# Kernel tuning notes

Hardware: AMD Instinct MI355X
Metric: run time of the kernel (lower is better)

Reference implementation:

```python
import jax, jax.numpy as jnp
import numpy as np

Q_HEADS, KV_HEADS, HEAD_DIM, WINDOW = 16, 4, 128, 512
HIDDEN = 2048
ROPE_BASE = 10000.0


def _rope_tables(T, head_dim, dtype):
    half = head_dim // 2
    inv_freq = 1.0 / (ROPE_BASE ** (jnp.arange(half, dtype=jnp.float32) / half))
    t = jnp.arange(T, dtype=jnp.float32)
    freqs = jnp.outer(t, inv_freq)  # [T, half]
    return jnp.cos(freqs).astype(dtype), jnp.sin(freqs).astype(dtype)


def _apply_rope(x, cos, sin):
    # x: [B, T, H, D]; cos/sin: [T, D//2] -> broadcast [1, T, 1, D//2]
    c = cos[None, :, None, :]
    s = sin[None, :, None, :]
    x1, x2 = jnp.split(x, 2, axis=-1)
    return jnp.concatenate([x1 * c - x2 * s, x1 * s + x2 * c], axis=-1)


def setup_inputs() -> dict:
    key = jax.random.key(0)
    ks = jax.random.split(key, 5)
    B, T = 1, 4096
    x = jax.random.normal(ks[0], (B, T, HIDDEN), dtype=jnp.float32)
    sc = 0.02
    wq = jax.random.normal(ks[1], (Q_HEADS * HEAD_DIM, HIDDEN), dtype=jnp.float32) * sc
    wk = jax.random.normal(ks[2], (KV_HEADS * HEAD_DIM, HIDDEN), dtype=jnp.float32) * sc
    wv = jax.random.normal(ks[3], (KV_HEADS * HEAD_DIM, HIDDEN), dtype=jnp.float32) * sc
    wo = jax.random.normal(ks[4], (HIDDEN, Q_HEADS * HEAD_DIM), dtype=jnp.float32) * sc
    return {"x": x, "wq": wq, "wk": wk, "wv": wv, "wo": wo}


def reference(x, wq, wk, wv, wo):
    B, T, _ = x.shape
    reps = Q_HEADS // KV_HEADS
    scale = 1.0 / np.sqrt(HEAD_DIM)

    q = jnp.einsum('bth,oh->bto', x, wq).reshape(B, T, Q_HEADS, HEAD_DIM)
    k = jnp.einsum('bth,oh->bto', x, wk).reshape(B, T, KV_HEADS, HEAD_DIM)
    v = jnp.einsum('bth,oh->bto', x, wv).reshape(B, T, KV_HEADS, HEAD_DIM)

    cos, sin = _rope_tables(T, HEAD_DIM, x.dtype)
    q = _apply_rope(q, cos, sin)
    k = _apply_rope(k, cos, sin)

    # GQA without materializing repeated K/V: group q as [B,T,KVH,reps,D]
    qg = q.reshape(B, T, KV_HEADS, reps, HEAD_DIM)
    scores = jnp.einsum('btgrd,bsgd->bgrts', qg, k) * scale  # [B,KVH,reps,T,T]

    idx = jnp.arange(T)
    # allowed: causal (s <= t) AND within window (t - s <= WINDOW)
    allowed = (idx[None, :] <= idx[:, None]) & (idx[:, None] - idx[None, :] <= WINDOW)
    scores = jnp.where(allowed[None, None, None], scores, jnp.finfo(scores.dtype).min)
    probs = jax.nn.softmax(scores, axis=-1)

    out = jnp.einsum('bgrts,bsgd->btgrd', probs, v)  # [B,T,KVH,reps,D]
    out = out.reshape(B, T, Q_HEADS * HEAD_DIM)
    return jnp.einsum('bto,ho->bth', out, wo)
```

## Files before the change

### kernel.cpp

```cpp
#include <hip/hip_runtime.h>

typedef __attribute__((ext_vector_type(8))) short short8;
typedef __attribute__((ext_vector_type(4))) short short4_t;
typedef __attribute__((ext_vector_type(4))) float f32x4;
typedef __attribute__((ext_vector_type(4))) unsigned short u16x4;

__device__ __forceinline__ unsigned short f2b(float f) {
  unsigned int u = __float_as_uint(f);
  u += 0x7fffu + ((u >> 16) & 1u);
  return (unsigned short)(u >> 16);
}
__device__ __forceinline__ float b2f(unsigned short s) {
  return __uint_as_float(((unsigned int)s) << 16);
}
__device__ __forceinline__ void glds16(const void* g, void* l) {
  __builtin_amdgcn_global_load_lds(
      (const __attribute__((address_space(1))) unsigned int*)g,
      (__attribute__((address_space(3))) unsigned int*)l, 16, 0, 0);
}

__global__ __launch_bounds__(256) void cast_all(const float* __restrict__ x,
                                                const float* __restrict__ wq,
                                                const float* __restrict__ wk,
                                                const float* __restrict__ wv,
                                                const float* __restrict__ wo,
                                                unsigned short* __restrict__ dst) {
  const int i = blockIdx.x * 256 + threadIdx.x;
  const float* s;
  int off;
  if (i < 2097152)      { s = x;  off = i; }
  else if (i < 3145728) { s = wq; off = i - 2097152; }
  else if (i < 3407872) { s = wk; off = i - 3145728; }
  else if (i < 3670016) { s = wv; off = i - 3407872; }
  else                  { s = wo; off = i - 3670016; }
  f32x4 v = ((const f32x4*)s)[off];
  u16x4 o;
  o[0] = f2b(v[0]); o[1] = f2b(v[1]); o[2] = f2b(v[2]); o[3] = f2b(v[3]);
  ((u16x4*)dst)[i] = o;
}

__global__ __launch_bounds__(256) void gemm_qkv(const unsigned short* __restrict__ A,
                                                const unsigned short* __restrict__ B,
                                                unsigned short* __restrict__ qb,
                                                unsigned short* __restrict__ kb,
                                                unsigned short* __restrict__ vtg) {
  const int K = 2048;
  __shared__ unsigned short As[128 * 32];
  __shared__ unsigned short Bs[128 * 32];
  const int tid = threadIdx.x;
  const int w = tid >> 6, lane = tid & 63;
  const int quad = lane >> 4, l15 = lane & 15;
  const int m0 = blockIdx.x * 128;
  const int nt = blockIdx.y;
  const int n0 = nt * 128;
  const int mbase = (w >> 1) * 64;
  const f32x4 fzero = {0.f, 0.f, 0.f, 0.f};

  f32x4 acc[4][4];
#pragma unroll
  for (int i = 0; i < 4; i++)
#pragma unroll
    for (int j = 0; j < 4; j++) acc[i][j] = fzero;

  const int srow = w * 16 + (lane >> 2);
  const int scol = (lane & 3) * 8;
  const unsigned short* Ag0 = A + (size_t)(m0 + srow) * K + scol;
  const unsigned short* Ag1 = Ag0 + (size_t)64 * K;
  const unsigned short* Bg0 = B + (size_t)(n0 + srow) * K + scol;
  const unsigned short* Bg1 = Bg0 + (size_t)64 * K;

  for (int k0 = 0; k0 < K; k0 += 32) {
    __syncthreads();
    glds16(Ag0 + k0, &As[w * 512]);
    glds16(Ag1 + k0, &As[2048 + w * 512]);
    glds16(Bg0 + k0, &Bs[w * 512]);
    glds16(Bg1 + k0, &Bs[2048 + w * 512]);
    __syncthreads();
    short8 af[4], bf[4];
#pragma unroll
    for (int mi = 0; mi < 4; mi++)
      af[mi] = *(const short8*)&As[(mbase + mi * 16 + l15) * 32 + quad * 8];
#pragma unroll
    for (int ni = 0; ni < 4; ni++) {
      const int ngrp = (w & 1) * 2 + (ni & 1) + (ni >> 1) * 4;
      bf[ni] = *(const short8*)&Bs[(ngrp * 16 + l15) * 32 + quad * 8];
    }
#pragma unroll
    for (int mi = 0; mi < 4; mi++)
#pragma unroll
      for (int ni = 0; ni < 4; ni++)
        acc[mi][ni] = __builtin_amdgcn_mfma_f32_16x16x32_bf16(af[mi], bf[ni], acc[mi][ni], 0, 0, 0);
  }

  if (nt >= 20) {
    const int g = nt - 20;
#pragma unroll
    for (int mi = 0; mi < 4; mi++) {
      const int tb = m0 + mbase + mi * 16 + quad * 4;
#pragma unroll
      for (int ni = 0; ni < 4; ni++) {
        const int d = ((w & 1) * 2 + (ni & 1) + (ni >> 1) * 4) * 16 + l15;
        u16x4 o;
#pragma unroll
        for (int r = 0; r < 4; r++) o[r] = f2b(acc[mi][ni][r]);
        *(u16x4*)(vtg + (size_t)(g * 128 + d) * 4096 + tb) = o;
      }
    }
  } else {
    unsigned short* dst;
    int stride, hoff;
    if (nt < 16) { dst = qb; stride = 2048; hoff = nt * 128; }
    else         { dst = kb; stride = 512;  hoff = (nt - 16) * 128; }
    const float c2 = 0.20762050593045889f;
    const float inv2pi = 0.15915494309189535f;
#pragma unroll
    for (int ni = 0; ni < 2; ni++) {
      const int i = (w & 1) * 32 + ni * 16 + l15;
      const float inv_rev = exp2f(-(float)i * c2) * inv2pi;
#pragma unroll
      for (int mi = 0; mi < 4; mi++) {
#pragma unroll
        for (int r = 0; r < 4; r++) {
          const int t = m0 + mbase + mi * 16 + quad * 4 + r;
          float rev = (float)t * inv_rev;
          rev = rev - floorf(rev);
          const float sn = __builtin_amdgcn_sinf(rev);
          const float cs = __builtin_amdgcn_cosf(rev);
          const float x1 = acc[mi][ni][r], x2 = acc[mi][ni + 2][r];
          unsigned short* p = dst + (size_t)t * stride + hoff + i;
          p[0]  = f2b(x1 * cs - x2 * sn);
          p[64] = f2b(x1 * sn + x2 * cs);
        }
      }
    }
  }
}

__global__ __launch_bounds__(256) void gemm_bt(const unsigned short* __restrict__ A,
                                               const unsigned short* __restrict__ B,
                                               float* __restrict__ Cout,
                                               int M, int N, int K) {
  __shared__ unsigned short As[128 * 32];
  __shared__ unsigned short Bs[128 * 32];
  const int tid = threadIdx.x;
  const int w = tid >> 6, lane = tid & 63;
  const int quad = lane >> 4, l15 = lane & 15;
  const int m0 = blockIdx.x * 128, n0 = blockIdx.y * 128;
  const int mbase = (w >> 1) * 64, nbase = (w & 1) * 64;
  const f32x4 fzero = {0.f, 0.f, 0.f, 0.f};

  f32x4 acc[4][4];
#pragma unroll
  for (int i = 0; i < 4; i++)
#pragma unroll
    for (int j = 0; j < 4; j++) acc[i][j] = fzero;

  const int srow = w * 16 + (lane >> 2);
  const int scol = (lane & 3) * 8;
  const unsigned short* Ag0 = A + (size_t)(m0 + srow) * K + scol;
  const unsigned short* Ag1 = Ag0 + (size_t)64 * K;
  const unsigned short* Bg0 = B + (size_t)(n0 + srow) * K + scol;
  const unsigned short* Bg1 = Bg0 + (size_t)64 * K;

  for (int k0 = 0; k0 < K; k0 += 32) {
    __syncthreads();
    glds16(Ag0 + k0, &As[w * 512]);
    glds16(Ag1 + k0, &As[2048 + w * 512]);
    glds16(Bg0 + k0, &Bs[w * 512]);
    glds16(Bg1 + k0, &Bs[2048 + w * 512]);
    __syncthreads();
    short8 af[4], bf[4];
#pragma unroll
    for (int mi = 0; mi < 4; mi++)
      af[mi] = *(const short8*)&As[(mbase + mi * 16 + l15) * 32 + quad * 8];
#pragma unroll
    for (int ni = 0; ni < 4; ni++)
      bf[ni] = *(const short8*)&Bs[(nbase + ni * 16 + l15) * 32 + quad * 8];
#pragma unroll
    for (int mi = 0; mi < 4; mi++)
#pragma unroll
      for (int ni = 0; ni < 4; ni++)
        acc[mi][ni] = __builtin_amdgcn_mfma_f32_16x16x32_bf16(af[mi], bf[ni], acc[mi][ni], 0, 0, 0);
  }

#pragma unroll
  for (int mi = 0; mi < 4; mi++)
#pragma unroll
    for (int ni = 0; ni < 4; ni++) {
      const int row = m0 + mbase + mi * 16 + quad * 4;
      const int col = n0 + nbase + ni * 16 + l15;
#pragma unroll
      for (int r = 0; r < 4; r++)
        Cout[(size_t)(row + r) * N + col] = acc[mi][ni][r];
    }
}

__global__ __launch_bounds__(512) void attn_fwd(const unsigned short* __restrict__ qp,
                                                const unsigned short* __restrict__ kp,
                                                const unsigned short* __restrict__ vtg,
                                                unsigned short* __restrict__ op) {
  __shared__ unsigned short Ks[2][4][1024];
  __shared__ unsigned short Vt[2][4096];
  const int tid = threadIdx.x;
  const int w = tid >> 6, lane = tid & 63;
  const int quad = lane >> 4, l15 = lane & 15;
  const int t0 = blockIdx.x * 64;
  const int g = blockIdx.y;
  const int h = g * 4 + (w & 3);
  const int t0w = t0 + (w >> 2) * 32;
  const f32x4 fzero = {0.f, 0.f, 0.f, 0.f};
  const float scale = 0.088388347648318447f;
  const float NEG_INF = -__builtin_inff();

  short8 qf[4][2];
#pragma unroll
  for (int qt = 0; qt < 2; qt++) {
    const unsigned short* qrow = qp + (size_t)(t0w + qt * 16 + l15) * 2048 + h * 128 + quad * 8;
#pragma unroll
    for (int kb = 0; kb < 4; kb++) qf[kb][qt] = *(const short8*)(qrow + kb * 32);
  }

  f32x4 oacc[8][2];
#pragma unroll
  for (int db = 0; db < 8; db++) { oacc[db][0] = fzero; oacc[db][1] = fzero; }
  float Mrow[2] = {-1.0e30f, -1.0e30f}, Lrow[2] = {0.f, 0.f};

  const int s_begin = (t0 >= 512) ? (t0 - 512) : 0;
  const int nch = ((t0 + 63 - s_begin) >> 5) + 1;

  const int r4 = lane >> 2, c4 = lane & 3;
#define ATTN_STAGE(s0_, b_)                                                              \
  {                                                                                      \
    const int s0v = (s0_);                                                               \
    if (w < 4) {                                                                         \
      _Pragma("unroll")                                                                  \
      for (int p = 0; p < 2; p++)                                                        \
        glds16(kp + (size_t)(s0v + p * 16 + r4) * 512 + g * 128 + w * 32 + c4 * 8,       \
               &Ks[b_][w][p * 512]);                                                     \
    } else {                                                                             \
      const int wv = w - 4;                                                              \
      _Pragma("unroll")                                                                  \
      for (int p = 0; p < 2; p++)                                                        \
        glds16(vtg + (size_t)(g * 128 + wv * 32 + p * 16 + r4) * 4096 + s0v + c4 * 8,    \
               &Vt[b_][wv * 1024 + p * 512]);                                            \
    }                                                                                    \
  }

  ATTN_STAGE(s_begin, 0);

  for (int c = 0; c < nch; ++c) {
    const int s0 = s_begin + c * 32;
    const int b = c & 1;
    __syncthreads();
    if (c + 1 < nch) ATTN_STAGE(s_begin + (c + 1) * 32, (c + 1) & 1);

    if (s0 + 31 >= t0w - 512 && s0 <= t0w + 31) {
      f32x4 sacc[2][2];
      sacc[0][0] = fzero; sacc[0][1] = fzero; sacc[1][0] = fzero; sacc[1][1] = fzero;
      const int permBase = ((l15 >> 2) << 3) + (l15 & 3);
#pragma unroll
      for (int kb = 0; kb < 4; kb++) {
        short8 af0 = *(const short8*)&Ks[b][kb][(permBase + 0) * 32 + quad * 8];
        short8 af1 = *(const short8*)&Ks[b][kb][(permBase + 4) * 32 + quad * 8];
        sacc[0][0] = __builtin_amdgcn_mfma_f32_16x16x32_bf16(af0, qf[kb][0], sacc[0][0], 0, 0, 0);
        sacc[0][1] = __builtin_amdgcn_mfma_f32_16x16x32_bf16(af0, qf[kb][1], sacc[0][1], 0, 0, 0);
        sacc[1][0] = __builtin_amdgcn_mfma_f32_16x16x32_bf16(af1, qf[kb][0], sacc[1][0], 0, 0, 0);
        sacc[1][1] = __builtin_amdgcn_mfma_f32_16x16x32_bf16(af1, qf[kb][1], sacc[1][1], 0, 0, 0);
      }

      short8 pb[2];
      float alpha[2];
#pragma unroll
      for (int qt = 0; qt < 2; qt++) {
        const int tq = t0w + qt * 16 + l15;
        float vals[8];
        float cmax = NEG_INF;
#pragma unroll
        for (int kt = 0; kt < 2; kt++)
#pragma unroll
          for (int r = 0; r < 4; r++) {
            const int s = s0 + quad * 8 + kt * 4 + r;
            const bool ok = (unsigned)(tq - s) <= 512u;
            const float v = ok ? sacc[kt][qt][r] * scale : NEG_INF;
            vals[kt * 4 + r] = v;
            cmax = fmaxf(cmax, v);
          }
        cmax = fmaxf(cmax, __shfl_xor(cmax, 16));
        cmax = fmaxf(cmax, __shfl_xor(cmax, 32));
        const float Mnew = fmaxf(Mrow[qt], cmax);
        alpha[qt] = __expf(Mrow[qt] - Mnew);
        Mrow[qt] = Mnew;
        float csum = 0.f;
#pragma unroll
        for (int j = 0; j < 8; j++) {
          const float p = __expf(vals[j] - Mnew);
          csum += p;
          pb[qt][j] = (short)f2b(p);
        }
        csum += __shfl_xor(csum, 16);
        csum += __shfl_xor(csum, 32);
        Lrow[qt] = Lrow[qt] * alpha[qt] + csum;
      }

#pragma unroll
      for (int db = 0; db < 8; db++) {
        short8 vf = *(const short8*)&Vt[b][(db * 16 + l15) * 32 + quad * 8];
#pragma unroll
        for (int qt = 0; qt < 2; qt++) {
          oacc[db][qt][0] *= alpha[qt]; oacc[db][qt][1] *= alpha[qt];
          oacc[db][qt][2] *= alpha[qt]; oacc[db][qt][3] *= alpha[qt];
          oacc[db][qt] = __builtin_amdgcn_mfma_f32_16x16x32_bf16(vf, pb[qt], oacc[db][qt], 0, 0, 0);
        }
      }
    }
  }
#undef ATTN_STAGE

#pragma unroll
  for (int qt = 0; qt < 2; qt++) {
    const float invL = 1.f / Lrow[qt];
    unsigned short* orow = op + (size_t)(t0w + qt * 16 + l15) * 2048 + h * 128;
#pragma unroll
    for (int db = 0; db < 8; db++) {
      u16x4 o;
#pragma unroll
      for (int r = 0; r < 4; r++) o[r] = f2b(oacc[db][qt][r] * invL);
      *(u16x4*)(orow + db * 16 + quad * 4) = o;
    }
  }
}

extern "C" void kernel_launch(void* const* d_in, const int* in_sizes, int n_in,
                              void* d_out, int out_size, void* d_ws, size_t ws_size,
                              hipStream_t stream) {
  const float* x  = (const float*)d_in[0];
  const float* wq = (const float*)d_in[1];
  const float* wk = (const float*)d_in[2];
  const float* wv = (const float*)d_in[3];
  const float* wo = (const float*)d_in[4];
  float* out = (float*)d_out;
  char* ws = (char*)d_ws;

  unsigned short* xb    = (unsigned short*)(ws + 0);
  unsigned short* wqkv  = (unsigned short*)(ws + 16777216);
  unsigned short* wob   = (unsigned short*)(ws + 29360128);
  unsigned short* qb    = (unsigned short*)(ws + 37748736);
  unsigned short* kbuf  = (unsigned short*)(ws + 54525952);
  unsigned short* vtg   = (unsigned short*)(ws + 58720256);
  unsigned short* attnb = xb;

  cast_all<<<18432, 256, 0, stream>>>(x, wq, wk, wv, wo, (unsigned short*)ws);

  gemm_qkv<<<dim3(32, 24), 256, 0, stream>>>(xb, wqkv, qb, kbuf, vtg);

  attn_fwd<<<dim3(64, 4), 512, 0, stream>>>(qb, kbuf, vtg, attnb);

  gemm_bt<<<dim3(32, 16), 256, 0, stream>>>(attnb, wob, out, 4096, 2048, 2048);
}
```

Baseline: 284.6 us.

## Replace both GEMMs with a 256x256 double-buffered, swizzled, prioritized MFMA kernel

The separate 128x128 QKV and output-projection GEMMs are replaced by one 256x256-tile, 512-thread kernel. It double-buffers 64-wide K slices in 128KB of dynamic LDS, XOR-swizzles the LDS layout to avoid bank conflicts, and interleaves global-to-LDS staging with MFMA quadrants using s_setprio and split barriers. The goal is to hide memory latency and raise data reuse per block. In exchange the grids shrink to 192 and 128 blocks, which may underfill the GPU's compute units, and register pressure rises with 32 accumulators per lane.

```diff
diff --git a/kernel.cpp b/kernel.cpp
--- a/kernel.cpp
+++ b/kernel.cpp
@@ -1,7 +1,6 @@
 #include <hip/hip_runtime.h>
 
 typedef __attribute__((ext_vector_type(8))) short short8;
-typedef __attribute__((ext_vector_type(4))) short short4_t;
 typedef __attribute__((ext_vector_type(4))) float f32x4;
 typedef __attribute__((ext_vector_type(4))) unsigned short u16x4;
 
@@ -9,9 +8,6 @@
   unsigned int u = __float_as_uint(f);
   u += 0x7fffu + ((u >> 16) & 1u);
   return (unsigned short)(u >> 16);
-}
-__device__ __forceinline__ float b2f(unsigned short s) {
-  return __uint_as_float(((unsigned int)s) << 16);
 }
 __device__ __forceinline__ void glds16(const void* g, void* l) {
   __builtin_amdgcn_global_load_lds(
@@ -39,94 +35,184 @@
   ((u16x4*)dst)[i] = o;
 }
 
-__global__ __launch_bounds__(256) void gemm_qkv(const unsigned short* __restrict__ A,
-                                                const unsigned short* __restrict__ B,
-                                                unsigned short* __restrict__ qb,
-                                                unsigned short* __restrict__ kb,
-                                                unsigned short* __restrict__ vtg) {
-  const int K = 2048;
-  __shared__ unsigned short As[128 * 32];
-  __shared__ unsigned short Bs[128 * 32];
+__global__ __launch_bounds__(512, 2) void gemm256(
+    const unsigned short* __restrict__ A, const unsigned short* __restrict__ B,
+    const int K, const int mode,
+    unsigned short* __restrict__ qb, unsigned short* __restrict__ kb,
+    unsigned short* __restrict__ vtg, float* __restrict__ Cout, const int N) {
+  extern __shared__ char smem[];
   const int tid = threadIdx.x;
   const int w = tid >> 6, lane = tid & 63;
   const int quad = lane >> 4, l15 = lane & 15;
-  const int m0 = blockIdx.x * 128;
-  const int nt = blockIdx.y;
-  const int n0 = nt * 128;
-  const int mbase = (w >> 1) * 64;
-  const f32x4 fzero = {0.f, 0.f, 0.f, 0.f};
-
-  f32x4 acc[4][4];
-#pragma unroll
-  for (int i = 0; i < 4; i++)
-#pragma unroll
-    for (int j = 0; j < 4; j++) acc[i][j] = fzero;
-
-  const int srow = w * 16 + (lane >> 2);
-  const int scol = (lane & 3) * 8;
-  const unsigned short* Ag0 = A + (size_t)(m0 + srow) * K + scol;
-  const unsigned short* Ag1 = Ag0 + (size_t)64 * K;
-  const unsigned short* Bg0 = B + (size_t)(n0 + srow) * K + scol;
-  const unsigned short* Bg1 = Bg0 + (size_t)64 * K;
-
-  for (int k0 = 0; k0 < K; k0 += 32) {
-    __syncthreads();
-    glds16(Ag0 + k0, &As[w * 512]);
-    glds16(Ag1 + k0, &As[2048 + w * 512]);
-    glds16(Bg0 + k0, &Bs[w * 512]);
-    glds16(Bg1 + k0, &Bs[2048 + w * 512]);
-    __syncthreads();
-    short8 af[4], bf[4];
-#pragma unroll
-    for (int mi = 0; mi < 4; mi++)
-      af[mi] = *(const short8*)&As[(mbase + mi * 16 + l15) * 32 + quad * 8];
-#pragma unroll
-    for (int ni = 0; ni < 4; ni++) {
-      const int ngrp = (w & 1) * 2 + (ni & 1) + (ni >> 1) * 4;
-      bf[ni] = *(const short8*)&Bs[(ngrp * 16 + l15) * 32 + quad * 8];
-    }
-#pragma unroll
-    for (int mi = 0; mi < 4; mi++)
-#pragma unroll
-      for (int ni = 0; ni < 4; ni++)
-        acc[mi][ni] = __builtin_amdgcn_mfma_f32_16x16x32_bf16(af[mi], bf[ni], acc[mi][ni], 0, 0, 0);
-  }
-
-  if (nt >= 20) {
-    const int g = nt - 20;
-#pragma unroll
-    for (int mi = 0; mi < 4; mi++) {
-      const int tb = m0 + mbase + mi * 16 + quad * 4;
-#pragma unroll
-      for (int ni = 0; ni < 4; ni++) {
-        const int d = ((w & 1) * 2 + (ni & 1) + (ni >> 1) * 4) * 16 + l15;
+  const int wm = w >> 2, wn = w & 3;
+  const int m0 = blockIdx.x * 256, n0 = blockIdx.y * 256;
+  const int nkt = K >> 6;
+
+  int nb[4];
+#pragma unroll
+  for (int ni = 0; ni < 4; ++ni) {
+    const int bbi = (wn & 1) * 4 + ni;
+    nb[ni] = mode ? ((bbi & 1) ? 4 + (bbi >> 1) : (bbi >> 1)) : bbi;
+  }
+
+  const int fragOff = l15 * 64 + ((quad * 16) ^ ((l15 & 8) << 2));
+  char* const aWave = smem + wm * 16384;
+  char* const bWave = smem + 32768 + (wn >> 1) * 16384;
+
+  const int sr = lane >> 2;
+  const int sc = ((lane & 3) * 8) ^ ((lane & 32) ? 16 : 0);
+
+  auto stageA = [&](int buf, int h, int kt) {
+#pragma unroll
+    for (int j = 0; j < 2; ++j) {
+      const int s = j * 8 + w;
+      glds16(A + (size_t)(m0 + h * 128 + (s >> 1) * 16 + sr) * K + kt * 64 + (s & 1) * 32 + sc,
+             smem + buf * 65536 + h * 16384 + s * 1024);
+    }
+  };
+  auto stageB = [&](int buf, int h, int kt) {
+#pragma unroll
+    for (int j = 0; j < 2; ++j) {
+      const int s = j * 8 + w;
+      glds16(B + (size_t)(n0 + h * 128 + (s >> 1) * 16 + sr) * K + kt * 64 + (s & 1) * 32 + sc,
+             smem + buf * 65536 + 32768 + h * 16384 + s * 1024);
+    }
+  };
+
+  f32x4 acc[8][4];
+  const f32x4 fz = {0.f, 0.f, 0.f, 0.f};
+#pragma unroll
+  for (int i = 0; i < 8; ++i)
+#pragma unroll
+    for (int j = 0; j < 4; ++j) acc[i][j] = fz;
+
+  stageB(0, 0, 0); stageA(0, 0, 0); stageA(0, 1, 0); stageB(0, 1, 0);
+  stageB(1, 0, 1); stageA(1, 0, 1);
+  asm volatile("s_waitcnt vmcnt(4)" ::: "memory");
+  __builtin_amdgcn_s_barrier();
+
+  short8 af[4][2], blo[2][2], bhi[2][2];
+
+#define MFMA_Q(MOFF, NOFF, BF)                                                   \
+  _Pragma("unroll") for (int mi = 0; mi < 4; ++mi)                               \
+  _Pragma("unroll") for (int ni = 0; ni < 2; ++ni)                               \
+  _Pragma("unroll") for (int kk = 0; kk < 2; ++kk)                               \
+      acc[(MOFF) + mi][(NOFF) + ni] = __builtin_amdgcn_mfma_f32_16x16x32_bf16(   \
+          af[mi][kk], BF[ni][kk], acc[(MOFF) + mi][(NOFF) + ni], 0, 0, 0);
+
+  for (int T = 0; T < nkt; ++T) {
+    const int c = T & 1;
+    char* const ab = aWave + c * 65536;
+    char* const bp = bWave + c * 65536;
+
+#pragma unroll
+    for (int mi = 0; mi < 4; ++mi)
+#pragma unroll
+      for (int kk = 0; kk < 2; ++kk)
+        af[mi][kk] = *(const short8*)(ab + (mi * 2 + kk) * 1024 + fragOff);
+#pragma unroll
+    for (int ni = 0; ni < 2; ++ni)
+#pragma unroll
+      for (int kk = 0; kk < 2; ++kk)
+        blo[ni][kk] = *(const short8*)(bp + (nb[ni] * 2 + kk) * 1024 + fragOff);
+    if (T + 1 < nkt) stageA(c ^ 1, 1, T + 1);
+    __builtin_amdgcn_s_barrier();
+    asm volatile("s_waitcnt lgkmcnt(0)" ::: "memory");
+    __builtin_amdgcn_s_setprio(1);
+    MFMA_Q(0, 0, blo)
+    __builtin_amdgcn_s_setprio(0);
+    __builtin_amdgcn_s_barrier();
+
+#pragma unroll
+    for (int ni = 0; ni < 2; ++ni)
+#pragma unroll
+      for (int kk = 0; kk < 2; ++kk)
+        bhi[ni][kk] = *(const short8*)(bp + (nb[ni + 2] * 2 + kk) * 1024 + fragOff);
+    if (T + 1 < nkt) stageB(c ^ 1, 1, T + 1);
+    __builtin_amdgcn_s_barrier();
+    asm volatile("s_waitcnt lgkmcnt(0)" ::: "memory");
+    __builtin_amdgcn_s_setprio(1);
+    MFMA_Q(0, 2, bhi)
+    __builtin_amdgcn_s_setprio(0);
+    __builtin_amdgcn_s_barrier();
+
+#pragma unroll
+    for (int mi = 0; mi < 4; ++mi)
+#pragma unroll
+      for (int kk = 0; kk < 2; ++kk)
+        af[mi][kk] = *(const short8*)(ab + ((mi + 4) * 2 + kk) * 1024 + fragOff);
+    if (T + 2 < nkt) stageB(c, 0, T + 2);
+    __builtin_amdgcn_s_barrier();
+    asm volatile("s_waitcnt lgkmcnt(0)" ::: "memory");
+    __builtin_amdgcn_s_setprio(1);
+    MFMA_Q(4, 2, bhi)
+    __builtin_amdgcn_s_setprio(0);
+    __builtin_amdgcn_s_barrier();
+
+    if (T + 2 < nkt) stageA(c, 0, T + 2);
+    __builtin_amdgcn_s_barrier();
+    __builtin_amdgcn_s_setprio(1);
+    MFMA_Q(4, 0, blo)
+    __builtin_amdgcn_s_setprio(0);
+    if (T + 2 < nkt) { asm volatile("s_waitcnt vmcnt(4)" ::: "memory"); }
+    else             { asm volatile("s_waitcnt vmcnt(0)" ::: "memory"); }
+    __builtin_amdgcn_s_barrier();
+  }
+#undef MFMA_Q
+
+  if (mode == 0) {
+    const int colBase = n0 + wn * 64;
+#pragma unroll
+    for (int mi = 0; mi < 8; ++mi) {
+      const int row = m0 + wm * 128 + mi * 16 + quad * 4;
+#pragma unroll
+      for (int ni = 0; ni < 4; ++ni) {
+        const int col = colBase + ni * 16 + l15;
+#pragma unroll
+        for (int r = 0; r < 4; ++r)
+          Cout[(size_t)(row + r) * N + col] = acc[mi][ni][r];
+      }
+    }
+    return;
+  }
+
+  const int y = blockIdx.y;
+  const int tb0 = m0 + wm * 128;
+  if (y >= 10) {
+    const int g = (y - 10) * 2 + (wn >> 1);
+#pragma unroll
+    for (int mi = 0; mi < 8; ++mi) {
+      const int tb = tb0 + mi * 16 + quad * 4;
+#pragma unroll
+      for (int ni = 0; ni < 4; ++ni) {
+        const int d = nb[ni] * 16 + l15;
         u16x4 o;
 #pragma unroll
-        for (int r = 0; r < 4; r++) o[r] = f2b(acc[mi][ni][r]);
+        for (int r = 0; r < 4; ++r) o[r] = f2b(acc[mi][ni][r]);
         *(u16x4*)(vtg + (size_t)(g * 128 + d) * 4096 + tb) = o;
       }
     }
   } else {
     unsigned short* dst;
     int stride, hoff;
-    if (nt < 16) { dst = qb; stride = 2048; hoff = nt * 128; }
-    else         { dst = kb; stride = 512;  hoff = (nt - 16) * 128; }
+    if (y < 8) { dst = qb; stride = 2048; hoff = (y * 2 + (wn >> 1)) * 128; }
+    else       { dst = kb; stride = 512;  hoff = ((y - 8) * 2 + (wn >> 1)) * 128; }
     const float c2 = 0.20762050593045889f;
     const float inv2pi = 0.15915494309189535f;
 #pragma unroll
-    for (int ni = 0; ni < 2; ni++) {
-      const int i = (w & 1) * 32 + ni * 16 + l15;
+    for (int j = 0; j < 2; ++j) {
+      const int i = ((wn & 1) * 2 + j) * 16 + l15;
       const float inv_rev = exp2f(-(float)i * c2) * inv2pi;
 #pragma unroll
-      for (int mi = 0; mi < 4; mi++) {
-#pragma unroll
-        for (int r = 0; r < 4; r++) {
-          const int t = m0 + mbase + mi * 16 + quad * 4 + r;
+      for (int mi = 0; mi < 8; ++mi) {
+#pragma unroll
+        for (int r = 0; r < 4; ++r) {
+          const int t = tb0 + mi * 16 + quad * 4 + r;
           float rev = (float)t * inv_rev;
-          rev = rev - floorf(rev);
+          rev -= floorf(rev);
           const float sn = __builtin_amdgcn_sinf(rev);
           const float cs = __builtin_amdgcn_cosf(rev);
-          const float x1 = acc[mi][ni][r], x2 = acc[mi][ni + 2][r];
+          const float x1 = acc[mi][2 * j][r], x2 = acc[mi][2 * j + 1][r];
           unsigned short* p = dst + (size_t)t * stride + hoff + i;
           p[0]  = f2b(x1 * cs - x2 * sn);
           p[64] = f2b(x1 * sn + x2 * cs);
@@ -134,65 +220,6 @@
       }
     }
   }
-}
-
-__global__ __launch_bounds__(256) void gemm_bt(const unsigned short* __restrict__ A,
-                                               const unsigned short* __restrict__ B,
-                                               float* __restrict__ Cout,
-                                               int M, int N, int K) {
-  __shared__ unsigned short As[128 * 32];
-  __shared__ unsigned short Bs[128 * 32];
-  const int tid = threadIdx.x;
-  const int w = tid >> 6, lane = tid & 63;
-  const int quad = lane >> 4, l15 = lane & 15;
-  const int m0 = blockIdx.x * 128, n0 = blockIdx.y * 128;
-  const int mbase = (w >> 1) * 64, nbase = (w & 1) * 64;
-  const f32x4 fzero = {0.f, 0.f, 0.f, 0.f};
-
-  f32x4 acc[4][4];
-#pragma unroll
-  for (int i = 0; i < 4; i++)
-#pragma unroll
-    for (int j = 0; j < 4; j++) acc[i][j] = fzero;
-
-  const int srow = w * 16 + (lane >> 2);
-  const int scol = (lane & 3) * 8;
-  const unsigned short* Ag0 = A + (size_t)(m0 + srow) * K + scol;
-  const unsigned short* Ag1 = Ag0 + (size_t)64 * K;
-  const unsigned short* Bg0 = B + (size_t)(n0 + srow) * K + scol;
-  const unsigned short* Bg1 = Bg0 + (size_t)64 * K;
-
-  for (int k0 = 0; k0 < K; k0 += 32) {
-    __syncthreads();
-    glds16(Ag0 + k0, &As[w * 512]);
-    glds16(Ag1 + k0, &As[2048 + w * 512]);
-    glds16(Bg0 + k0, &Bs[w * 512]);
-    glds16(Bg1 + k0, &Bs[2048 + w * 512]);
-    __syncthreads();
-    short8 af[4], bf[4];
-#pragma unroll
-    for (int mi = 0; mi < 4; mi++)
-      af[mi] = *(const short8*)&As[(mbase + mi * 16 + l15) * 32 + quad * 8];
-#pragma unroll
-    for (int ni = 0; ni < 4; ni++)
-      bf[ni] = *(const short8*)&Bs[(nbase + ni * 16 + l15) * 32 + quad * 8];
-#pragma unroll
-    for (int mi = 0; mi < 4; mi++)
-#pragma unroll
-      for (int ni = 0; ni < 4; ni++)
-        acc[mi][ni] = __builtin_amdgcn_mfma_f32_16x16x32_bf16(af[mi], bf[ni], acc[mi][ni], 0, 0, 0);
-  }
-
-#pragma unroll
-  for (int mi = 0; mi < 4; mi++)
-#pragma unroll
-    for (int ni = 0; ni < 4; ni++) {
-      const int row = m0 + mbase + mi * 16 + quad * 4;
-      const int col = n0 + nbase + ni * 16 + l15;
-#pragma unroll
-      for (int r = 0; r < 4; r++)
-        Cout[(size_t)(row + r) * N + col] = acc[mi][ni][r];
-    }
 }
 
 __global__ __launch_bounds__(512) void attn_fwd(const unsigned short* __restrict__ qp,
@@ -349,11 +376,20 @@
   unsigned short* vtg   = (unsigned short*)(ws + 58720256);
   unsigned short* attnb = xb;
 
+  static bool attr_done = false;
+  if (!attr_done) {
+    hipFuncSetAttribute(reinterpret_cast<const void*>(gemm256),
+                        hipFuncAttributeMaxDynamicSharedMemorySize, 131072);
+    attr_done = true;
+  }
+
   cast_all<<<18432, 256, 0, stream>>>(x, wq, wk, wv, wo, (unsigned short*)ws);
 
-  gemm_qkv<<<dim3(32, 24), 256, 0, stream>>>(xb, wqkv, qb, kbuf, vtg);
+  gemm256<<<dim3(16, 12), 512, 131072, stream>>>(xb, wqkv, 2048, 1,
+                                                 qb, kbuf, vtg, nullptr, 0);
 
   attn_fwd<<<dim3(64, 4), 512, 0, stream>>>(qb, kbuf, vtg, attnb);
 
-  gemm_bt<<<dim3(32, 16), 256, 0, stream>>>(attnb, wob, out, 4096, 2048, 2048);
-}
+  gemm256<<<dim3(16, 8), 512, 131072, stream>>>(attnb, wob, 2048, 0,
+                                                nullptr, nullptr, nullptr, out, 2048);
+}
```

After: 274.3 us. 1.04x faster.
